# Optimization experiments

Hardware: AMD Instinct MI355X
Metric: run time of the kernel (lower is better)

## Reference

```python
import jax, jax.numpy as jnp
import numpy as np


def setup_inputs() -> dict:
    key = jax.random.key(0)
    k1, k2, k3, k4 = jax.random.split(key, 4)
    B, Cin, Cout, K, Wd, H, Wsp = 16, 256, 256, 3, 256, 64, 64
    fan_in = Cin * K * K
    return {
        "x": jax.random.normal(k1, (B, Cin, H, Wsp), dtype=jnp.float32),
        "w": jax.random.normal(k2, (B, Wd), dtype=jnp.float32),
        "conv_weight": jax.random.normal(k3, (Cout, Cin, K, K), dtype=jnp.float32) * 0.05,
        "style_w": jax.random.normal(k4, (Cin, Wd), dtype=jnp.float32) * 0.05,
        "style_b": jnp.zeros((Cin,), dtype=jnp.float32),
        "scale": jnp.asarray(1.0 / np.sqrt(fan_in), dtype=jnp.float32),
    }


def reference(x, w, conv_weight, style_w, style_b, scale):
    # x: [B, Cin, H, W]; w: [B, Wd]; conv_weight: [Cout, Cin, K, K]
    B, Cin, H, Wsp = x.shape
    Cout, _, K, _ = conv_weight.shape
    # style modulation: s = Linear(w) -> [B, 1, Cin, 1, 1]
    s = (w @ style_w.T + style_b).reshape(B, 1, Cin, 1, 1)
    # modulate + demodulate per-sample weights: [B, Cout, Cin, K, K]
    wt = (conv_weight * scale)[None] * s
    demod = jax.lax.rsqrt(jnp.sum(wt * wt, axis=(2, 3, 4), keepdims=True) + 1e-8)
    wt = (wt * demod).reshape(B * Cout, Cin, K, K)
    # grouped conv emulation: input [1, B*Cin, H, W], groups=B
    xr = x.reshape(1, B * Cin, H, Wsp)
    pad = 1
    out = jax.lax.conv_general_dilated(
        xr, wt,
        window_strides=(1, 1),
        padding=[(pad, pad), (pad, pad)],
        dimension_numbers=("NCHW", "OIHW", "NCHW"),
        feature_group_count=B,
    )
    return out.reshape(B, Cout, out.shape[2], out.shape[3])
```

## Files before the change

kernel.cpp:

```cpp
#include <hip/hip_runtime.h>
#include <hip/hip_bf16.h>

#define BB   16
#define CIN  256
#define COUT 256
#define WD   256
#define HH   64
#define WWS  64
#define NSP  4096
#define KW   9

typedef __attribute__((ext_vector_type(8))) short short8;
typedef __attribute__((ext_vector_type(4))) float f32x4;
typedef unsigned short ushort_t;

#define S_BYTES (BB*CIN*4)
#define WT_OFF (S_BYTES)
#define WT_BYTES (BB*9*COUT*CIN*2)
#define X_OFF (WT_OFF + WT_BYTES)
#define X_BYTES (BB*NSP*CIN*2)
#define ZP_OFF (X_OFF + X_BYTES)
#define ZP_BYTES 4096
#define WS_NEEDED ((size_t)(ZP_OFF + ZP_BYTES))

#define WAITVM1 asm volatile("s_waitcnt vmcnt(1)" ::: "memory")
#define WAITVM4 asm volatile("s_waitcnt vmcnt(4)" ::: "memory")

__device__ inline ushort_t f2bf(float f) {
    __hip_bfloat16 h = __float2bfloat16(f);
    return __builtin_bit_cast(ushort_t, h);
}

__device__ inline void gload_lds16(const ushort_t* g, ushort_t* l) {
    __builtin_amdgcn_global_load_lds(
        (const __attribute__((address_space(1))) void*)g,
        (__attribute__((address_space(3))) void*)l, 16, 0, 0);
}

__global__ __launch_bounds__(256)
void zero_kernel(float* __restrict__ zp) {
    ((float4*)zp)[threadIdx.x] = make_float4(0.f, 0.f, 0.f, 0.f);
}

__global__ __launch_bounds__(256)
void style_kernel(const float* __restrict__ w,
                  const float* __restrict__ style_w,
                  const float* __restrict__ style_b,
                  float* __restrict__ s) {
    const int b  = blockIdx.x;
    const int ci = threadIdx.x;
    __shared__ float wsh[WD];
    wsh[ci] = w[b * WD + ci];
    __syncthreads();
    const float* row = style_w + ci * WD;
    float acc = style_b[ci];
    #pragma unroll 4
    for (int k = 0; k < WD; ++k) acc += wsh[k] * row[k];
    s[b * CIN + ci] = acc;
}

__global__ __launch_bounds__(256)
void wt_kernel(const float* __restrict__ cw, const float* __restrict__ s,
               const float* __restrict__ scale_p, ushort_t* __restrict__ wt) {
    const int co = blockIdx.x, b = blockIdx.y, ci = threadIdx.x;
    const float sv = s[b * CIN + ci] * scale_p[0];
    const float* cp = cw + ((size_t)co * CIN + ci) * KW;
    float v[9];
    float ss = 0.f;
    #pragma unroll
    for (int t = 0; t < 9; ++t) { v[t] = cp[t] * sv; ss += v[t] * v[t]; }
    #pragma unroll
    for (int off = 32; off > 0; off >>= 1) ss += __shfl_down(ss, off);
    __shared__ float red[4];
    if ((ci & 63) == 0) red[ci >> 6] = ss;
    __syncthreads();
    const float dm = rsqrtf(red[0] + red[1] + red[2] + red[3] + 1e-8f);
    #pragma unroll
    for (int t = 0; t < 9; ++t)
        wt[((size_t)(b * 9 + t) * COUT + co) * CIN + ci] = f2bf(v[t] * dm);
}

__global__ __launch_bounds__(256)
void xpose_kernel(const float* __restrict__ x, ushort_t* __restrict__ xo) {
    const int spt = blockIdx.x;
    const int cit = blockIdx.y;
    const int b   = blockIdx.z;
    const int t   = threadIdx.x;
    __shared__ ushort_t tile[64 * 68];
    const int sp0 = spt * 64, ci0 = cit * 64;
    {
        const int spq = t & 15, cil = t >> 4;
        #pragma unroll
        for (int i = 0; i < 4; ++i) {
            const int ci = cil + i * 16;
            const float4 v = *(const float4*)(x + ((size_t)(b * CIN + ci0 + ci)) * NSP + sp0 + spq * 4);
            tile[(spq * 4 + 0) * 68 + ci] = f2bf(v.x);
            tile[(spq * 4 + 1) * 68 + ci] = f2bf(v.y);
            tile[(spq * 4 + 2) * 68 + ci] = f2bf(v.z);
            tile[(spq * 4 + 3) * 68 + ci] = f2bf(v.w);
        }
    }
    __syncthreads();
    {
        const int g4 = t & 15, sp = t >> 4;
        #pragma unroll
        for (int i = 0; i < 4; ++i) {
            const int spp = sp + i * 16;
            uint2 v = *(const uint2*)&tile[spp * 68 + g4 * 4];
            *(uint2*)(xo + ((size_t)(b * NSP + sp0 + spp)) * CIN + ci0 + g4 * 4) = v;
        }
    }
}

__global__ __launch_bounds__(512, 4)
void conv_mfma_kernel(const ushort_t* __restrict__ wt,
                      const ushort_t* __restrict__ xo,
                      const ushort_t* __restrict__ zp,
                      float* __restrict__ out) {
    const int wg = blockIdx.x;
    const int b  = (wg & 7) | (((wg >> 3) & 1) << 3);
    const int r2 = wg >> 4;
    const int cohalf = r2 & 1;
    const int ntile  = r2 >> 1;
    const int y0 = ntile * 4;

    const int tid  = threadIdx.x;
    const int lane = tid & 63;
    const int w    = tid >> 6;
    const int wm   = w >> 2;
    const int wn   = w & 3;
    const int l15  = lane & 15;
    const int lg   = lane >> 4;
    const int q    = lane >> 2;

    __shared__ __align__(16) ushort_t lds_a[3 * 128 * 32];
    __shared__ __align__(16) ushort_t lds_x[2 * 6 * 66 * 32];

    const int srcqA8 = ((lane & 3) ^ ((q ^ (q >> 2)) & 3)) * 8;
    const long wtb = (long)b * 9 * COUT * CIN;
    const ushort_t* pa = wt + wtb + (long)(cohalf * 128 + w * 16 + q) * CIN + srcqA8;
    const int aluni = w * 512;

    const ushort_t* px[3];
    int xdst_off[3];
    #pragma unroll
    for (int j = 0; j < 3; ++j) {
        const int idx = j * 8 + w;
        const int r   = idx >> 2;
        const int cg  = idx & 3;
        const int col = cg * 16 + (lane >> 2);
        const int sq8 = ((lane & 3) ^ ((col ^ (col >> 2)) & 3)) * 8;
        const int y   = y0 - 1 + r;
        const bool val = (y >= 0 && y < HH);
        px[j] = val ? (xo + ((long)b * NSP + (long)y * WWS + col) * CIN + sq8)
                    : (zp + lane * 8);
        xdst_off[j] = r * 2112 + (cg * 16 + 1) * 32;
    }

    const int slotA8 = (lg ^ ((l15 ^ (l15 >> 2)) & 3)) * 8;
    int slotB8[3];
    #pragma unroll
    for (int kx = 0; kx < 3; ++kx) {
        int c2 = l15 + kx - 1;
        if (c2 < 0) c2 = 0;
        slotB8[kx] = (lg ^ ((c2 ^ (c2 >> 2)) & 3)) * 8;
    }
    const int abase = (wm * 64 + l15) * 32 + slotA8;

    f32x4 acc[4][4];
    #pragma unroll
    for (int mi = 0; mi < 4; ++mi)
        #pragma unroll
        for (int ni = 0; ni < 4; ++ni) acc[mi][ni] = (f32x4){0.f, 0.f, 0.f, 0.f};

    if (tid < 96) {
        const int cell = tid >> 2, qq = tid & 3;
        const int buf = cell / 12, cr = cell % 12;
        const int r = cr >> 1, col = (cr & 1) * 65;
        *(uint4*)&lds_x[buf * 12672 + r * 2112 + col * 32 + qq * 8] =
            make_uint4(0, 0, 0, 0);
    }
    asm volatile("s_waitcnt lgkmcnt(0)" ::: "memory");
    __builtin_amdgcn_sched_barrier(0);

    #pragma unroll
    for (int j = 0; j < 3; ++j)
        gload_lds16(px[j], lds_x + xdst_off[j]);
    gload_lds16(pa, lds_a + aluni);
    gload_lds16(pa + (long)COUT * CIN, lds_a + 4096 + aluni);

    for (int chunk = 0; chunk < 8; ++chunk) {
        const ushort_t* xb = lds_x + (chunk & 1) * 12672;

        #pragma unroll
        for (int tap = 0; tap < 9; ++tap) {
            if (tap == 1 || tap == 2) { WAITVM4; } else { WAITVM1; }
            __builtin_amdgcn_sched_barrier(0);
            __builtin_amdgcn_s_barrier();

            {
                const int tp2 = (tap + 2) % 9;
                const int ch2 = (tap >= 7) ? ((chunk + 1) & 7) : chunk;
                const long aoff = (long)tp2 * (COUT * CIN) + ch2 * 32;
                gload_lds16(pa + aoff, lds_a + ((tap + 2) % 3) * 4096 + aluni);
            }
            if (tap == 0) {
                const int cs = (chunk + 1) & 7;
                ushort_t* xdst = lds_x + ((chunk + 1) & 1) * 12672;
                #pragma unroll
                for (int j = 0; j < 3; ++j)
                    gload_lds16(px[j] + cs * 32, xdst + xdst_off[j]);
            }

            const int ky = tap / 3, kx = tap % 3;
            const ushort_t* ab = lds_a + (tap % 3) * 4096 + abase;
            short8 af[4];
            #pragma unroll
            for (int mi = 0; mi < 4; ++mi) af[mi] = *(const short8*)(ab + mi * 512);
            short8 bf[4];
            #pragma unroll
            for (int ni = 0; ni < 4; ++ni) {
                const int row = wn + ky;
                const int col = ni * 16 + l15 + kx;
                bf[ni] = *(const short8*)(xb + row * 2112 + col * 32 + slotB8[kx]);
            }

            __builtin_amdgcn_s_setprio(1);
            #pragma unroll
            for (int mi = 0; mi < 4; ++mi)
                #pragma unroll
                for (int ni = 0; ni < 4; ++ni)
                    acc[mi][ni] = __builtin_amdgcn_mfma_f32_16x16x32_bf16(
                        bf[ni], af[mi], acc[mi][ni], 0, 0, 0);
            __builtin_amdgcn_s_setprio(0);
        }
    }

    #pragma unroll
    for (int mi = 0; mi < 4; ++mi) {
        const int co = cohalf * 128 + wm * 64 + mi * 16 + l15;
        float* ob = out + ((long)(b * COUT + co)) * NSP
                  + ntile * 256 + wn * 64 + lg * 4;
        #pragma unroll
        for (int ni = 0; ni < 4; ++ni)
            *(f32x4*)(ob + ni * 16) = acc[mi][ni];
    }
}

__global__ __launch_bounds__(256)
void modconv_kernel(const float* __restrict__ x,
                    const float* __restrict__ cw,
                    const float* __restrict__ s,
                    const float* __restrict__ scale_p,
                    float* __restrict__ out) {
    const int tile = blockIdx.x;
    const int co   = blockIdx.y;
    const int b    = blockIdx.z;
    const int tid  = threadIdx.x;
    const float scale = scale_p[0];

    __shared__ float s_wt[CIN * KW];
    __shared__ float s_x[18 * 66];
    __shared__ float red[4];

    const float* cwb = cw + (size_t)co * CIN * KW;
    const float* sb  = s + b * CIN;
    float sumsq = 0.f;
    for (int i = tid; i < CIN * KW; i += 256) {
        float v = cwb[i] * scale * sb[i / KW];
        s_wt[i] = v;
        sumsq += v * v;
    }
    #pragma unroll
    for (int off = 32; off > 0; off >>= 1) sumsq += __shfl_down(sumsq, off);
    if ((tid & 63) == 0) red[tid >> 6] = sumsq;
    __syncthreads();
    const float demod = rsqrtf(red[0] + red[1] + red[2] + red[3] + 1e-8f);
    for (int i = tid; i < CIN * KW; i += 256) s_wt[i] *= demod;

    const int tx = tid & 63;
    const int tr = tid >> 6;
    const int y0 = tile * 16;
    float acc[4] = {0.f, 0.f, 0.f, 0.f};

    for (int ci = 0; ci < CIN; ++ci) {
        __syncthreads();
        const float* xb = x + ((size_t)(b * CIN + ci)) * (HH * WWS);
        for (int idx = tid; idx < 18 * 66; idx += 256) {
            const int r = idx / 66, c = idx % 66;
            const int yg = y0 - 1 + r, xg = c - 1;
            float v = 0.f;
            if (yg >= 0 && yg < HH && xg >= 0 && xg < WWS) v = xb[yg * WWS + xg];
            s_x[idx] = v;
        }
        __syncthreads();
        const float* wr = s_wt + ci * KW;
        const float w0 = wr[0], w1 = wr[1], w2 = wr[2];
        const float w3 = wr[3], w4 = wr[4], w5 = wr[5];
        const float w6 = wr[6], w7 = wr[7], w8 = wr[8];
        const int rbase = tr * 4;
        float xv[6][3];
        #pragma unroll
        for (int j = 0; j < 6; ++j)
            #pragma unroll
            for (int k = 0; k < 3; ++k) xv[j][k] = s_x[(rbase + j) * 66 + tx + k];
        #pragma unroll
        for (int i = 0; i < 4; ++i)
            acc[i] += w0 * xv[i][0] + w1 * xv[i][1] + w2 * xv[i][2]
                    + w3 * xv[i+1][0] + w4 * xv[i+1][1] + w5 * xv[i+1][2]
                    + w6 * xv[i+2][0] + w7 * xv[i+2][1] + w8 * xv[i+2][2];
    }
    float* ob = out + (((size_t)(b * COUT + co)) * HH + y0) * WWS + tx;
    #pragma unroll
    for (int i = 0; i < 4; ++i) ob[(tr * 4 + i) * WWS] = acc[i];
}

extern "C" void kernel_launch(void* const* d_in, const int* in_sizes, int n_in,
                              void* d_out, int out_size, void* d_ws, size_t ws_size,
                              hipStream_t stream) {
    const float* x       = (const float*)d_in[0];
    const float* w       = (const float*)d_in[1];
    const float* cw      = (const float*)d_in[2];
    const float* style_w = (const float*)d_in[3];
    const float* style_b = (const float*)d_in[4];
    const float* scale_p = (const float*)d_in[5];
    float*       out     = (float*)d_out;

    float*    s    = (float*)d_ws;
    ushort_t* wswt = (ushort_t*)((char*)d_ws + WT_OFF);
    ushort_t* wsx  = (ushort_t*)((char*)d_ws + X_OFF);
    float*    zp   = (float*)((char*)d_ws + ZP_OFF);

    style_kernel<<<dim3(BB), 256, 0, stream>>>(w, style_w, style_b, s);

    if (ws_size >= WS_NEEDED) {
        zero_kernel<<<dim3(1), 256, 0, stream>>>(zp);
        wt_kernel<<<dim3(COUT, BB), 256, 0, stream>>>(cw, s, scale_p, wswt);
        xpose_kernel<<<dim3(64, 4, BB), 256, 0, stream>>>(x, wsx);
        conv_mfma_kernel<<<dim3(512), 512, 0, stream>>>(wswt, wsx,
                                                        (const ushort_t*)zp, out);
    } else {
        modconv_kernel<<<dim3(4, COUT, BB), 256, 0, stream>>>(x, cw, s, scale_p, out);
    }
}
```

Baseline: 110.3 us.

## Enlarge conv tile to full Cout per block with tap-row grouped pipeline

Each workgroup of the MFMA conv now computes all 256 output channels for a 4-row spatial tile instead of half, so the staged input tile is reused across twice as many channels and the grid halves to 256 blocks. Weight staging moves from one tap per barrier to three taps (one kernel row) per barrier, double-buffered, which cuts barriers per chunk from nine to three. Each wave now holds a 4x8 accumulator tile and launch bounds drop to 2 blocks per CU. The cost is much larger LDS for weights, higher register pressure, and fewer blocks than CUs, which may leave compute units idle.

```diff
diff --git a/kernel.cpp b/kernel.cpp
--- a/kernel.cpp
+++ b/kernel.cpp
@@ -13,6 +13,7 @@
 typedef __attribute__((ext_vector_type(8))) short short8;
 typedef __attribute__((ext_vector_type(4))) float f32x4;
 typedef unsigned short ushort_t;
+typedef unsigned int uint_t;
 
 #define S_BYTES (BB*CIN*4)
 #define WT_OFF (S_BYTES)
@@ -23,8 +24,8 @@
 #define ZP_BYTES 4096
 #define WS_NEEDED ((size_t)(ZP_OFF + ZP_BYTES))
 
-#define WAITVM1 asm volatile("s_waitcnt vmcnt(1)" ::: "memory")
-#define WAITVM4 asm volatile("s_waitcnt vmcnt(4)" ::: "memory")
+#define WAITVM0 asm volatile("s_waitcnt vmcnt(0)" ::: "memory")
+#define WAITVM3 asm volatile("s_waitcnt vmcnt(3)" ::: "memory")
 
 __device__ inline ushort_t f2bf(float f) {
     __hip_bfloat16 h = __float2bfloat16(f);
@@ -112,49 +113,44 @@
     }
 }
 
-__global__ __launch_bounds__(512, 4)
+__global__ __launch_bounds__(512, 2)
 void conv_mfma_kernel(const ushort_t* __restrict__ wt,
                       const ushort_t* __restrict__ xo,
                       const ushort_t* __restrict__ zp,
                       float* __restrict__ out) {
-    const int wg = blockIdx.x;
-    const int b  = (wg & 7) | (((wg >> 3) & 1) << 3);
-    const int r2 = wg >> 4;
-    const int cohalf = r2 & 1;
-    const int ntile  = r2 >> 1;
-    const int y0 = ntile * 4;
+    const int wg    = blockIdx.x;
+    const int b     = wg & 15;
+    const int ntile = wg >> 4;
+    const int y0    = ntile * 4;
 
     const int tid  = threadIdx.x;
     const int lane = tid & 63;
     const int w    = tid >> 6;
-    const int wm   = w >> 2;
-    const int wn   = w & 3;
+    const int wm   = w >> 1;
+    const int wn   = w & 1;
     const int l15  = lane & 15;
     const int lg   = lane >> 4;
-    const int q    = lane >> 2;
-
-    __shared__ __align__(16) ushort_t lds_a[3 * 128 * 32];
+
+    __shared__ __align__(16) ushort_t lds_a[2 * 3 * 256 * 32];
     __shared__ __align__(16) ushort_t lds_x[2 * 6 * 66 * 32];
 
-    const int srcqA8 = ((lane & 3) ^ ((q ^ (q >> 2)) & 3)) * 8;
-    const long wtb = (long)b * 9 * COUT * CIN;
-    const ushort_t* pa = wt + wtb + (long)(cohalf * 128 + w * 16 + q) * CIN + srcqA8;
-    const int aluni = w * 512;
-
+    const int keyW  = ((lane >> 2) ^ (lane >> 4)) & 3;
+    const uint_t srcq8 = (uint_t)(((lane & 3) ^ keyW) * 8);
+
+    const uint_t wtb    = (uint_t)b * 9u * COUT * CIN;
+    const uint_t a_src0 = (uint_t)(tid >> 2) * 256u + srcq8;
+    const int    tid8   = tid * 8;
+
+    const int hi  = tid >> 8;
+    const int col = (tid >> 2) & 63;
+    const int xdb = hi * 2112 + (col + 1) * 32 + (lane & 3) * 8;
     const ushort_t* px[3];
-    int xdst_off[3];
     #pragma unroll
     for (int j = 0; j < 3; ++j) {
-        const int idx = j * 8 + w;
-        const int r   = idx >> 2;
-        const int cg  = idx & 3;
-        const int col = cg * 16 + (lane >> 2);
-        const int sq8 = ((lane & 3) ^ ((col ^ (col >> 2)) & 3)) * 8;
-        const int y   = y0 - 1 + r;
-        const bool val = (y >= 0 && y < HH);
-        px[j] = val ? (xo + ((long)b * NSP + (long)y * WWS + col) * CIN + sq8)
-                    : (zp + lane * 8);
-        xdst_off[j] = r * 2112 + (cg * 16 + 1) * 32;
+        const int y = y0 - 1 + hi + 2 * j;
+        px[j] = (y >= 0 && y < HH)
+              ? (xo + (uint_t)b * (NSP * CIN) + (uint_t)(y * WWS + col) * CIN + srcq8)
+              : (zp + lane * 8);
     }
 
     const int slotA8 = (lg ^ ((l15 ^ (l15 >> 2)) & 3)) * 8;
@@ -167,84 +163,104 @@
     }
     const int abase = (wm * 64 + l15) * 32 + slotA8;
 
-    f32x4 acc[4][4];
+    f32x4 acc[4][8];
     #pragma unroll
     for (int mi = 0; mi < 4; ++mi)
         #pragma unroll
-        for (int ni = 0; ni < 4; ++ni) acc[mi][ni] = (f32x4){0.f, 0.f, 0.f, 0.f};
+        for (int ni = 0; ni < 8; ++ni) acc[mi][ni] = (f32x4){0.f, 0.f, 0.f, 0.f};
 
     if (tid < 96) {
         const int cell = tid >> 2, qq = tid & 3;
         const int buf = cell / 12, cr = cell % 12;
-        const int r = cr >> 1, col = (cr & 1) * 65;
-        *(uint4*)&lds_x[buf * 12672 + r * 2112 + col * 32 + qq * 8] =
+        const int r = cr >> 1, hc = (cr & 1) * 65;
+        *(uint4*)&lds_x[buf * 12672 + r * 2112 + hc * 32 + qq * 8] =
             make_uint4(0, 0, 0, 0);
     }
     asm volatile("s_waitcnt lgkmcnt(0)" ::: "memory");
     __builtin_amdgcn_sched_barrier(0);
 
-    #pragma unroll
-    for (int j = 0; j < 3; ++j)
-        gload_lds16(px[j], lds_x + xdst_off[j]);
-    gload_lds16(pa, lds_a + aluni);
-    gload_lds16(pa + (long)COUT * CIN, lds_a + 4096 + aluni);
-
+    #define ISSUE_A(TB, CHN, DSTSEL)                                           \
+    {   ushort_t* adst_ = lds_a + (DSTSEL) * 24576;                            \
+        _Pragma("unroll")                                                      \
+        for (int i_ = 0; i_ < 6; ++i_)                                         \
+            gload_lds16(wt + (wtb + (uint_t)((TB) + (i_ >> 1)) * 65536u        \
+                              + (uint_t)(CHN) * 32u + a_src0                   \
+                              + (uint_t)(i_ & 1) * 32768u),                    \
+                        adst_ + tid8 + i_ * 4096);                             \
+    }
+    #define ISSUE_X(CS, DSTSEL)                                                \
+    {   ushort_t* xdst_ = lds_x + (DSTSEL) * 12672;                            \
+        _Pragma("unroll")                                                      \
+        for (int j_ = 0; j_ < 3; ++j_)                                         \
+            gload_lds16(px[j_] + (CS) * 32, xdst_ + xdb + j_ * 4224);          \
+    }
+    #define READF(AF, BF, TG)                                                  \
+    {   _Pragma("unroll")                                                      \
+        for (int mi_ = 0; mi_ < 4; ++mi_)                                      \
+            AF[mi_] = *(const short8*)(ab + (TG) * 8192 + mi_ * 512);          \
+        _Pragma("unroll")                                                      \
+        for (int ni_ = 0; ni_ < 8; ++ni_)                                      \
+            BF[ni_] = *(const short8*)(xb + (xrow + (ni_ >> 2)) * 2112         \
+                        + ((ni_ & 3) * 16 + l15 + (TG)) * 32 + slotB8[TG]);    \
+    }
+    #define MFMAC(AF, BF)                                                      \
+    {   __builtin_amdgcn_s_setprio(1);                                         \
+        _Pragma("unroll")                                                      \
+        for (int mi_ = 0; mi_ < 4; ++mi_)                                      \
+            _Pragma("unroll")                                                  \
+            for (int ni_ = 0; ni_ < 8; ++ni_)                                  \
+                acc[mi_][ni_] = __builtin_amdgcn_mfma_f32_16x16x32_bf16(       \
+                    BF[ni_], AF[mi_], acc[mi_][ni_], 0, 0, 0);                 \
+        __builtin_amdgcn_s_setprio(0);                                         \
+    }
+
+    ISSUE_X(0, 0);
+    ISSUE_A(0, 0, 0);
+
+    #pragma unroll 1
     for (int chunk = 0; chunk < 8; ++chunk) {
-        const ushort_t* xb = lds_x + (chunk & 1) * 12672;
-
-        #pragma unroll
-        for (int tap = 0; tap < 9; ++tap) {
-            if (tap == 1 || tap == 2) { WAITVM4; } else { WAITVM1; }
+        #pragma unroll
+        for (int gph = 0; gph < 3; ++gph) {
+            if (gph == 2 && chunk != 7) { WAITVM3; } else { WAITVM0; }
             __builtin_amdgcn_sched_barrier(0);
             __builtin_amdgcn_s_barrier();
-
-            {
-                const int tp2 = (tap + 2) % 9;
-                const int ch2 = (tap >= 7) ? ((chunk + 1) & 7) : chunk;
-                const long aoff = (long)tp2 * (COUT * CIN) + ch2 * 32;
-                gload_lds16(pa + aoff, lds_a + ((tap + 2) % 3) * 4096 + aluni);
+            __builtin_amdgcn_sched_barrier(0);
+
+            const int Gpar = (chunk ^ gph) & 1;
+            if (!(chunk == 7 && gph == 2)) {
+                const int tb2 = ((gph + 1) % 3) * 3;
+                const int chn = chunk + (gph == 2 ? 1 : 0);
+                ISSUE_A(tb2, chn, Gpar ^ 1);
             }
-            if (tap == 0) {
-                const int cs = (chunk + 1) & 7;
-                ushort_t* xdst = lds_x + ((chunk + 1) & 1) * 12672;
-                #pragma unroll
-                for (int j = 0; j < 3; ++j)
-                    gload_lds16(px[j] + cs * 32, xdst + xdst_off[j]);
-            }
-
-            const int ky = tap / 3, kx = tap % 3;
-            const ushort_t* ab = lds_a + (tap % 3) * 4096 + abase;
-            short8 af[4];
-            #pragma unroll
-            for (int mi = 0; mi < 4; ++mi) af[mi] = *(const short8*)(ab + mi * 512);
-            short8 bf[4];
-            #pragma unroll
-            for (int ni = 0; ni < 4; ++ni) {
-                const int row = wn + ky;
-                const int col = ni * 16 + l15 + kx;
-                bf[ni] = *(const short8*)(xb + row * 2112 + col * 32 + slotB8[kx]);
-            }
-
-            __builtin_amdgcn_s_setprio(1);
-            #pragma unroll
-            for (int mi = 0; mi < 4; ++mi)
-                #pragma unroll
-                for (int ni = 0; ni < 4; ++ni)
-                    acc[mi][ni] = __builtin_amdgcn_mfma_f32_16x16x32_bf16(
-                        bf[ni], af[mi], acc[mi][ni], 0, 0, 0);
-            __builtin_amdgcn_s_setprio(0);
+            if (gph == 1 && chunk < 7) ISSUE_X(chunk + 1, (chunk + 1) & 1);
+
+            const ushort_t* ab = lds_a + Gpar * 24576 + abase;
+            const ushort_t* xb = lds_x + (chunk & 1) * 12672;
+            const int xrow = wn * 2 + gph;
+
+            short8 af0[4], bf0[8], af1[4], bf1[8];
+            READF(af0, bf0, 0);
+            READF(af1, bf1, 1);
+            MFMAC(af0, bf0);
+            READF(af0, bf0, 2);
+            MFMAC(af1, bf1);
+            MFMAC(af0, bf0);
         }
     }
 
     #pragma unroll
     for (int mi = 0; mi < 4; ++mi) {
-        const int co = cohalf * 128 + wm * 64 + mi * 16 + l15;
+        const int co = wm * 64 + mi * 16 + l15;
         float* ob = out + ((long)(b * COUT + co)) * NSP
-                  + ntile * 256 + wn * 64 + lg * 4;
-        #pragma unroll
-        for (int ni = 0; ni < 4; ++ni)
+                  + ntile * 256 + wn * 128 + lg * 4;
+        #pragma unroll
+        for (int ni = 0; ni < 8; ++ni)
             *(f32x4*)(ob + ni * 16) = acc[mi][ni];
     }
+    #undef ISSUE_A
+    #undef ISSUE_X
+    #undef READF
+    #undef MFMAC
 }
 
 __global__ __launch_bounds__(256)
@@ -337,7 +353,7 @@
         zero_kernel<<<dim3(1), 256, 0, stream>>>(zp);
         wt_kernel<<<dim3(COUT, BB), 256, 0, stream>>>(cw, s, scale_p, wswt);
         xpose_kernel<<<dim3(64, 4, BB), 256, 0, stream>>>(x, wsx);
-        conv_mfma_kernel<<<dim3(512), 512, 0, stream>>>(wswt, wsx,
+        conv_mfma_kernel<<<dim3(256), 512, 0, stream>>>(wswt, wsx,
                                                         (const ushort_t*)zp, out);
     } else {
         modconv_kernel<<<dim3(4, COUT, BB), 256, 0, stream>>>(x, cw, s, scale_p, out);
```

Measured after the change: 123.6 us. +12.1%, slower.
